# Performance work log

Hardware: AMD Instinct MI355X
Metric: run time of the kernel (lower is better)

## Reference

```python
import jax, jax.numpy as jnp
import numpy as np

N_NODES = 20000
N_EDGES = 640000
IN_NODE = 128
IN_EDGE = 16
HIDDEN = 64
OUT = 128
HEADS = 4
N_GRAPHS = 64
NEG_SLOPE = 0.2


def _glorot(key, shape):
    fan_in, fan_out = shape[0], shape[-1]
    s = jnp.sqrt(6.0 / (fan_in + fan_out)).astype(jnp.float32)
    return jax.random.uniform(key, shape, jnp.float32, -s, s)


def setup_inputs() -> dict:
    key = jax.random.key(0)
    ks = jax.random.split(key, 32)
    inp = {
        "x": jax.random.normal(ks[0], (N_NODES, IN_NODE), jnp.float32),
        "edge_attr": jax.random.normal(ks[1], (N_EDGES, IN_EDGE), jnp.float32),
        "edge_index": jax.random.randint(ks[2], (2, N_EDGES), 0, N_NODES),
        "batch": jnp.sort(jax.random.randint(ks[3], (N_NODES,), 0, N_GRAPHS)),
    }
    # layer dims: (in, out_per_head, concat)
    dims = [(IN_NODE, HIDDEN, True), (HIDDEN * HEADS, HIDDEN, True), (HIDDEN * HEADS, OUT, False)]
    k = 4
    for i, (cin, cout, concat) in enumerate(dims):
        hc = HEADS * cout
        inp[f"Wl{i}"] = _glorot(ks[k], (cin, hc)); k += 1
        inp[f"bl{i}"] = jnp.zeros((hc,), jnp.float32)
        inp[f"Wr{i}"] = _glorot(ks[k], (cin, hc)); k += 1
        inp[f"br{i}"] = jnp.zeros((hc,), jnp.float32)
        inp[f"We{i}"] = _glorot(ks[k], (IN_EDGE, hc)); k += 1
        inp[f"att{i}"] = _glorot(ks[k], (HEADS, cout)); k += 1
        inp[f"bias{i}"] = jnp.zeros((hc if concat else cout,), jnp.float32)
    return inp


def _gatv2_layer(x, edge_index, edge_attr, Wl, bl, Wr, br, We, att, bias, concat):
    """One PyG-style GATv2Conv layer with edge features."""
    H, C = att.shape
    N = x.shape[0]
    src, dst = edge_index[0], edge_index[1]
    xl = (x @ Wl + bl).reshape(N, H, C)  # messages from source
    xr = (x @ Wr + br).reshape(N, H, C)  # target query
    e = (edge_attr @ We).reshape(-1, H, C)
    m = jax.nn.leaky_relu(xl[src] + xr[dst] + e, NEG_SLOPE)  # [E,H,C]
    logits = jnp.einsum("ehc,hc->eh", m, att)  # [E,H]
    # scatter-softmax over edges grouped by destination node
    lmax = jax.ops.segment_max(logits, dst, num_segments=N)
    p = jnp.exp(logits - lmax[dst])
    denom = jax.ops.segment_sum(p, dst, num_segments=N)
    alpha = p / (denom[dst] + 1e-16)  # [E,H]
    out = jax.ops.segment_sum(alpha[:, :, None] * xl[src], dst, num_segments=N)  # [N,H,C]
    if concat:
        return out.reshape(N, H * C) + bias
    return out.mean(axis=1) + bias


def reference(x, edge_attr, edge_index, batch,
              Wl0, bl0, Wr0, br0, We0, att0, bias0,
              Wl1, bl1, Wr1, br1, We1, att1, bias1,
              Wl2, bl2, Wr2, br2, We2, att2, bias2):
    layers = [
        (Wl0, bl0, Wr0, br0, We0, att0, bias0, True),
        (Wl1, bl1, Wr1, br1, We1, att1, bias1, True),
        (Wl2, bl2, Wr2, br2, We2, att2, bias2, False),
    ]
    h = x
    for (Wl, bl, Wr, br, We, att, b, concat) in layers:
        h = _gatv2_layer(h, edge_index, edge_attr, Wl, bl, Wr, br, We, att, b, concat)
    # global max + mean pooling per graph
    x_max = jax.ops.segment_max(h, batch, num_segments=N_GRAPHS)
    s = jax.ops.segment_sum(h, batch, num_segments=N_GRAPHS)
    cnt = jax.ops.segment_sum(jnp.ones((h.shape[0], 1), h.dtype), batch, num_segments=N_GRAPHS)
    x_mean = s / jnp.maximum(cnt, 1.0)
    return jnp.concatenate([x_max, x_mean], axis=1)  # [G, 2*OUT]
```

## Files before the change

### kernel.cpp

```cpp
#include <hip/hip_runtime.h>

#define NB 8

__device__ __forceinline__ unsigned fmap(float f) {
  unsigned u = __float_as_uint(f);
  return (u & 0x80000000u) ? ~u : (u | 0x80000000u);
}
__device__ __forceinline__ float funmap(unsigned m) {
  unsigned u = (m & 0x80000000u) ? (m ^ 0x80000000u) : ~m;
  return __uint_as_float(u);
}

template <int K, int M>
__global__ __launch_bounds__(256) void node_gemm(
    const float* __restrict__ X, const float* __restrict__ W,
    const float* __restrict__ bias, float* __restrict__ Y) {
  constexpr int NPB = 16;
  constexpr int COLS4 = M / 4;
  constexpr int NG = 256 / COLS4;
  constexpr int RPN = NPB / NG;
  __shared__ float xs[NPB * K];
  const int tid = threadIdx.x;
  const int n0 = blockIdx.x * NPB;
  {
    const float4* X4 = reinterpret_cast<const float4*>(X + (size_t)n0 * K);
    float4* xs4 = reinterpret_cast<float4*>(xs);
    for (int i = tid; i < NPB * K / 4; i += 256) xs4[i] = X4[i];
  }
  __syncthreads();
  const int c4 = (tid % COLS4) * 4;
  const int r0 = (tid / COLS4) * RPN;
  float acc[RPN][4];
#pragma unroll
  for (int r = 0; r < RPN; ++r)
#pragma unroll
    for (int q = 0; q < 4; ++q) acc[r][q] = 0.f;

  for (int k = 0; k < K; k += 4) {
    float xv[RPN][4];
#pragma unroll
    for (int r = 0; r < RPN; ++r)
      *reinterpret_cast<float4*>(xv[r]) =
          *reinterpret_cast<const float4*>(&xs[(r0 + r) * K + k]);
#pragma unroll
    for (int j = 0; j < 4; ++j) {
      float wv[4];
      *reinterpret_cast<float4*>(wv) =
          *reinterpret_cast<const float4*>(&W[(size_t)(k + j) * M + c4]);
#pragma unroll
      for (int r = 0; r < RPN; ++r)
#pragma unroll
        for (int q = 0; q < 4; ++q)
          acc[r][q] = fmaf(xv[r][j], wv[q], acc[r][q]);
    }
  }
  float bv[4];
  *reinterpret_cast<float4*>(bv) = *reinterpret_cast<const float4*>(&bias[c4]);
#pragma unroll
  for (int r = 0; r < RPN; ++r) {
    float o[4];
#pragma unroll
    for (int q = 0; q < 4; ++q) o[q] = acc[r][q] + bv[q];
    *reinterpret_cast<float4*>(&Y[(size_t)(n0 + r0 + r) * M + c4]) =
        *reinterpret_cast<float4*>(o);
  }
}

__global__ void hist_b(const int* __restrict__ ei, int* __restrict__ kcnt,
                       int E, int bdiv) {
  int i = blockIdx.x * blockDim.x + threadIdx.x;
  if (i < E) atomicAdd(&kcnt[ei[E + i] * NB + ei[i] / bdiv], 1);
}

__global__ __launch_bounds__(1024) void blk_scan(
    const int* __restrict__ in, int* __restrict__ out1, int* __restrict__ bsum, int n) {
  __shared__ int buf[1024];
  const int tid = threadIdx.x;
  const int gid = blockIdx.x * 1024 + tid;
  int v = (gid < n) ? in[gid] : 0;
  buf[tid] = v;
  __syncthreads();
  for (int off = 1; off < 1024; off <<= 1) {
    int t = (tid >= off) ? buf[tid - off] : 0;
    __syncthreads();
    buf[tid] += t;
    __syncthreads();
  }
  if (gid < n) out1[gid] = buf[tid];
  if (tid == 1023) bsum[blockIdx.x] = buf[1023];
}

__global__ void scan_bsum(int* __restrict__ bsum, int nb) {
  if (blockIdx.x == 0 && threadIdx.x == 0) {
    int a = 0;
    for (int i = 0; i < nb; ++i) { a += bsum[i]; bsum[i] = a; }
  }
}

__global__ void add_off(int* __restrict__ kptr, const int* __restrict__ bsum, int n) {
  int gid = blockIdx.x * blockDim.x + threadIdx.x;
  if (gid == 0) kptr[0] = 0;
  if (gid < n) {
    int blk = gid >> 10;
    if (blk > 0) kptr[1 + gid] += bsum[blk - 1];
  }
}

__global__ void csr_fill_b(const int* __restrict__ ei, const int* __restrict__ kptr,
                           int* __restrict__ kfill, int* __restrict__ csr_src,
                           int* __restrict__ csr_eid, int E, int bdiv) {
  int i = blockIdx.x * blockDim.x + threadIdx.x;
  if (i < E) {
    int src = ei[i], dst = ei[E + i];
    int key = dst * NB + src / bdiv;
    int slot = kptr[key] + atomicAdd(&kfill[key], 1);
    csr_src[slot] = src;
    csr_eid[slot] = i;
  }
}

__global__ void ea_perm(const float* __restrict__ ea, const int* __restrict__ csr_eid,
                        float* __restrict__ ea_csr, int E) {
  int i = blockIdx.x * blockDim.x + threadIdx.x;
  if (i < E * 16) {
    int slot = i >> 4;
    ea_csr[i] = ea[((size_t)csr_eid[slot] << 4) + (i & 15)];
  }
}

template <int GS>
__device__ __forceinline__ void gat_edge_s(
    const float4 a, const float (&c)[16], const float4 xv,
    const float (&wef)[16][4], const float (&attv)[4],
    float& m, float& s, float (&acc)[4]) {
  float mv[4] = {a.x + xv.x, a.y + xv.y, a.z + xv.z, a.w + xv.w};
#pragma unroll
  for (int k = 0; k < 16; ++k) {
#pragma unroll
    for (int q = 0; q < 4; ++q) mv[q] = fmaf(c[k], wef[k][q], mv[q]);
  }
  float l = 0.f;
#pragma unroll
  for (int q = 0; q < 4; ++q) {
    const float v = fmaxf(mv[q], 0.2f * mv[q]);
    l = fmaf(v, attv[q], l);
  }
#pragma unroll
  for (int off = 1; off < GS; off <<= 1) l += __shfl_xor(l, off);
  const float nm = fmaxf(m, l);
  const float sc = __expf(m - nm);
  const float pe = __expf(l - nm);
  m = nm;
  s = fmaf(s, sc, pe);
  acc[0] = fmaf(pe, a.x, acc[0] * sc);
  acc[1] = fmaf(pe, a.y, acc[1] * sc);
  acc[2] = fmaf(pe, a.z, acc[2] * sc);
  acc[3] = fmaf(pe, a.w, acc[3] * sc);
}

template <int HCROW, int MODE>
__global__ __launch_bounds__(256) void fused_gat(
    const float* __restrict__ xl, const float* __restrict__ xr,
    const float* __restrict__ ea_csr, const float* __restrict__ We,
    const float* __restrict__ att, const float* __restrict__ bias,
    const int* __restrict__ kptr, const int* __restrict__ csr_src,
    float* __restrict__ out, int N, int colbase) {
  constexpr int C = HCROW / 4;
  constexpr int GS = C / 4;
  const int lane = threadIdx.x & 63;
  const int wslot = threadIdx.x >> 6;
  const int dst = blockIdx.x * 4 + wslot;
  if (dst >= N) return;

  float wef[16][4];
#pragma unroll
  for (int k = 0; k < 16; ++k)
    *reinterpret_cast<float4*>(wef[k]) =
        *reinterpret_cast<const float4*>(&We[k * HCROW + colbase + lane * 4]);
  const int col0 = colbase + lane * 4;
  const int head = col0 / C;
  float attv[4];
  *reinterpret_cast<float4*>(attv) =
      *reinterpret_cast<const float4*>(&att[head * C + (col0 % C)]);
  const float4* xl4 = reinterpret_cast<const float4*>(xl);
  const int rs4 = HCROW / 4;
  const int coff = col0 >> 2;
  const float4 xrv =
      reinterpret_cast<const float4*>(xr)[(size_t)dst * rs4 + coff];

  const int row0 = __builtin_amdgcn_readfirstlane(kptr[dst * NB]);
  const int rend = __builtin_amdgcn_readfirstlane(kptr[dst * NB + NB]);

  float m = -__builtin_inff(), s = 0.f;
  float acc[4] = {0.f, 0.f, 0.f, 0.f};

  if (row0 < rend) {
    const int last = rend - 1;
    const int s0 = csr_src[row0];
    const int s1 = csr_src[min(row0 + 1, last)];
    const int s2 = csr_src[min(row0 + 2, last)];
    const int s3 = csr_src[min(row0 + 3, last)];
    float4 a0 = xl4[(size_t)s0 * rs4 + coff];
    float4 a1 = xl4[(size_t)s1 * rs4 + coff];
    float4 a2 = xl4[(size_t)s2 * rs4 + coff];
    float4 a3 = xl4[(size_t)s3 * rs4 + coff];
    int sr0 = csr_src[min(row0 + 4, last)];
    int sr1 = csr_src[min(row0 + 5, last)];
    float c0[16], c1[16];
    {
      const float* e0 = ea_csr + (size_t)row0 * 16;
      const float* e1 = ea_csr + (size_t)min(row0 + 1, last) * 16;
#pragma unroll
      for (int k = 0; k < 16; ++k) { c0[k] = e0[k]; c1[k] = e1[k]; }
    }

    for (int p = row0; p < rend; p += 2) {
      const float4 na0 = xl4[(size_t)sr0 * rs4 + coff];
      const float4 na1 = xl4[(size_t)sr1 * rs4 + coff];
      const int nsr0 = csr_src[min(p + 6, last)];
      const int nsr1 = csr_src[min(p + 7, last)];
      float cn0[16], cn1[16];
      {
        const float* e0 = ea_csr + (size_t)min(p + 2, last) * 16;
        const float* e1 = ea_csr + (size_t)min(p + 3, last) * 16;
#pragma unroll
        for (int k = 0; k < 16; ++k) { cn0[k] = e0[k]; cn1[k] = e1[k]; }
      }
      gat_edge_s<GS>(a0, c0, xrv, wef, attv, m, s, acc);
      if (p + 1 < rend) gat_edge_s<GS>(a1, c1, xrv, wef, attv, m, s, acc);
      a0 = a2; a1 = a3; a2 = na0; a3 = na1;
      sr0 = nsr0; sr1 = nsr1;
#pragma unroll
      for (int k = 0; k < 16; ++k) { c0[k] = cn0[k]; c1[k] = cn1[k]; }
    }
  }

  const float inv = 1.f / (s + 1e-16f);
  float o[4];
  if (MODE == 0) {
    float bv[4];
    *reinterpret_cast<float4*>(bv) = *reinterpret_cast<const float4*>(&bias[col0]);
#pragma unroll
    for (int q = 0; q < 4; ++q) o[q] = fmaf(acc[q], inv, bv[q]);
    *reinterpret_cast<float4*>(&out[(size_t)dst * HCROW + col0]) =
        *reinterpret_cast<float4*>(o);
  } else {
#pragma unroll
    for (int q = 0; q < 4; ++q) {
      o[q] = acc[q] * inv;
      o[q] += __shfl_xor(o[q], 32);
    }
    if (lane < 32)
      *reinterpret_cast<float4*>(&out[(size_t)dst * 128 + lane * 4]) =
          *reinterpret_cast<float4*>(o);
  }
}

__global__ void pool_scatter(const float* __restrict__ hA, const float* __restrict__ hB,
                             const float* __restrict__ bias2, const int* __restrict__ batch,
                             unsigned* __restrict__ pmax, float* __restrict__ psum,
                             float* __restrict__ cnt, int N) {
  int idx = blockIdx.x * blockDim.x + threadIdx.x;
  if (idx >= N * 128) return;
  int n = idx >> 7, c = idx & 127;
  int g = batch[n];
  float v = 0.25f * (hA[idx] + hB[idx]) + bias2[c];
  atomicMax(&pmax[g * 128 + c], fmap(v));
  atomicAdd(&psum[g * 128 + c], v);
  if (c == 0) atomicAdd(&cnt[g], 1.f);
}

__global__ void pool_final(const unsigned* __restrict__ pmax, const float* __restrict__ psum,
                           const float* __restrict__ cnt, float* __restrict__ out) {
  int idx = blockIdx.x * blockDim.x + threadIdx.x;
  if (idx >= 64 * 128) return;
  int g = idx >> 7, c = idx & 127;
  float cg = cnt[g];
  out[g * 256 + c] = (cg > 0.f) ? funmap(pmax[idx]) : 0.f;
  out[g * 256 + 128 + c] = psum[idx] / fmaxf(cg, 1.f);
}

extern "C" void kernel_launch(void* const* d_in, const int* in_sizes, int n_in,
                              void* d_out, int out_size, void* d_ws, size_t ws_size,
                              hipStream_t stream) {
  const float* x     = (const float*)d_in[0];
  const float* ea    = (const float*)d_in[1];
  const int*   ei    = (const int*)d_in[2];
  const int*   batch = (const int*)d_in[3];
  const int N = in_sizes[0] / 128;
  const int E = in_sizes[2] / 2;
  const int NBINS = N * NB;
  const int bdiv = (N + NB - 1) / NB;

  const float* Wl[3]   = {(const float*)d_in[4],  (const float*)d_in[11], (const float*)d_in[18]};
  const float* blv[3]  = {(const float*)d_in[5],  (const float*)d_in[12], (const float*)d_in[19]};
  const float* Wr[3]   = {(const float*)d_in[6],  (const float*)d_in[13], (const float*)d_in[20]};
  const float* brv[3]  = {(const float*)d_in[7],  (const float*)d_in[14], (const float*)d_in[21]};
  const float* Wev[3]  = {(const float*)d_in[8],  (const float*)d_in[15], (const float*)d_in[22]};
  const float* attv[3] = {(const float*)d_in[9],  (const float*)d_in[16], (const float*)d_in[23]};
  const float* bias[3] = {(const float*)d_in[10], (const float*)d_in[17], (const float*)d_in[24]};

  float* ws = (float*)d_ws;
  float* xl     = ws;
  float* xr     = xl + (size_t)N * 512;
  float* ea_csr = xr + (size_t)N * 512;
  float* h      = ea_csr + (size_t)E * 16;
  int* kptr     = (int*)(h + (size_t)N * 256);
  int* csr_src  = kptr + (NBINS + 1);
  int* bsum     = csr_src + E;
  unsigned* pmax = (unsigned*)(bsum + 257);
  float* psum   = (float*)(pmax + 64 * 128);
  float* cnt    = psum + 64 * 128;
  int* csr_eid = (int*)h;
  int* kcnt    = csr_eid + E;
  int* kfill   = kcnt + NBINS;
  float* hsumA = h;
  float* hsumB = h + (size_t)N * 128;
  (void)n_in; (void)out_size; (void)ws_size;

  const int nodeBlocks = N / 16;
  const int edgeBlocks = (E + 255) / 256;
  const int scanBlocks = (NBINS + 1023) / 1024;
  const int gatBlocks = (N + 3) / 4;

  hipMemsetAsync(kcnt, 0, (size_t)2 * NBINS * sizeof(int), stream);
  hist_b<<<edgeBlocks, 256, 0, stream>>>(ei, kcnt, E, bdiv);
  blk_scan<<<scanBlocks, 1024, 0, stream>>>(kcnt, kptr + 1, bsum, NBINS);
  scan_bsum<<<1, 64, 0, stream>>>(bsum, scanBlocks);
  add_off<<<(NBINS + 255) / 256, 256, 0, stream>>>(kptr, bsum, NBINS);
  csr_fill_b<<<edgeBlocks, 256, 0, stream>>>(ei, kptr, kfill, csr_src, csr_eid, E, bdiv);
  ea_perm<<<(E * 16 + 255) / 256, 256, 0, stream>>>(ea, csr_eid, ea_csr, E);

  node_gemm<128, 256><<<nodeBlocks, 256, 0, stream>>>(x, Wl[0], blv[0], xl);
  node_gemm<128, 256><<<nodeBlocks, 256, 0, stream>>>(x, Wr[0], brv[0], xr);
  fused_gat<256, 0><<<gatBlocks, 256, 0, stream>>>(
      xl, xr, ea_csr, Wev[0], attv[0], bias[0], kptr, csr_src, h, N, 0);

  node_gemm<256, 256><<<nodeBlocks, 256, 0, stream>>>(h, Wl[1], blv[1], xl);
  node_gemm<256, 256><<<nodeBlocks, 256, 0, stream>>>(h, Wr[1], brv[1], xr);
  fused_gat<256, 0><<<gatBlocks, 256, 0, stream>>>(
      xl, xr, ea_csr, Wev[1], attv[1], bias[1], kptr, csr_src, h, N, 0);

  node_gemm<256, 512><<<nodeBlocks, 256, 0, stream>>>(h, Wl[2], blv[2], xl);
  node_gemm<256, 512><<<nodeBlocks, 256, 0, stream>>>(h, Wr[2], brv[2], xr);
  fused_gat<512, 1><<<gatBlocks, 256, 0, stream>>>(
      xl, xr, ea_csr, Wev[2], attv[2], bias[2], kptr, csr_src, hsumA, N, 0);
  fused_gat<512, 1><<<gatBlocks, 256, 0, stream>>>(
      xl, xr, ea_csr, Wev[2], attv[2], bias[2], kptr, csr_src, hsumB, N, 256);

  hipMemsetAsync(pmax, 0, (size_t)(64 * 128 * 2 + 64) * sizeof(float), stream);
  pool_scatter<<<(N * 128 + 255) / 256, 256, 0, stream>>>(hsumA, hsumB, bias[2], batch,
                                                          pmax, psum, cnt, N);
  pool_final<<<(64 * 128 + 255) / 256, 256, 0, stream>>>(pmax, psum, cnt, (float*)d_out);
}
```

Before: 1.119 ms.

## Replace atomic pooling with per-graph segmented reduction and merge final GAT launches

Per-node atomic max/sum pooling is replaced by a per-graph reduction. A small kernel finds each graph's node range from the sorted batch array, then one block per graph reduces its contiguous rows. This removes heavy atomic contention on 64x128 targets and drops the pool_final launch. The two column-half launches of the last GAT layer are also merged into one grid of twice the size. The pooling relies on batch being sorted, and 64 blocks give limited parallelism for the reduction.

```diff
diff --git a/kernel.cpp b/kernel.cpp
--- a/kernel.cpp
+++ b/kernel.cpp
@@ -1,15 +1,6 @@
 #include <hip/hip_runtime.h>
 
 #define NB 8
-
-__device__ __forceinline__ unsigned fmap(float f) {
-  unsigned u = __float_as_uint(f);
-  return (u & 0x80000000u) ? ~u : (u | 0x80000000u);
-}
-__device__ __forceinline__ float funmap(unsigned m) {
-  unsigned u = (m & 0x80000000u) ? (m ^ 0x80000000u) : ~m;
-  return __uint_as_float(u);
-}
 
 template <int K, int M>
 __global__ __launch_bounds__(256) void node_gemm(
@@ -128,6 +119,16 @@
   }
 }
 
+__global__ void graph_bounds(const int* __restrict__ batch, int* __restrict__ gstart,
+                             int* __restrict__ gend, int N) {
+  int i = blockIdx.x * blockDim.x + threadIdx.x;
+  if (i < N) {
+    int g = batch[i];
+    atomicMin(&gstart[g], i);
+    atomicMax(&gend[g], i + 1);
+  }
+}
+
 template <int GS>
 __device__ __forceinline__ void gat_edge_s(
     const float4 a, const float (&c)[16], const float4 xv,
@@ -164,12 +165,19 @@
     const float* __restrict__ ea_csr, const float* __restrict__ We,
     const float* __restrict__ att, const float* __restrict__ bias,
     const int* __restrict__ kptr, const int* __restrict__ csr_src,
-    float* __restrict__ out, int N, int colbase) {
+    float* __restrict__ out, float* __restrict__ outB, int N) {
   constexpr int C = HCROW / 4;
   constexpr int GS = C / 4;
   const int lane = threadIdx.x & 63;
   const int wslot = threadIdx.x >> 6;
-  const int dst = blockIdx.x * 4 + wslot;
+  int bx = blockIdx.x;
+  int colbase = 0;
+  float* o_ptr = out;
+  if (MODE == 1) {
+    const int gb = gridDim.x >> 1;
+    if (bx >= gb) { bx -= gb; colbase = 256; o_ptr = outB; }
+  }
+  const int dst = bx * 4 + wslot;
   if (dst >= N) return;
 
   float wef[16][4];
@@ -242,7 +250,7 @@
     *reinterpret_cast<float4*>(bv) = *reinterpret_cast<const float4*>(&bias[col0]);
 #pragma unroll
     for (int q = 0; q < 4; ++q) o[q] = fmaf(acc[q], inv, bv[q]);
-    *reinterpret_cast<float4*>(&out[(size_t)dst * HCROW + col0]) =
+    *reinterpret_cast<float4*>(&o_ptr[(size_t)dst * HCROW + col0]) =
         *reinterpret_cast<float4*>(o);
   } else {
 #pragma unroll
@@ -251,33 +259,36 @@
       o[q] += __shfl_xor(o[q], 32);
     }
     if (lane < 32)
-      *reinterpret_cast<float4*>(&out[(size_t)dst * 128 + lane * 4]) =
+      *reinterpret_cast<float4*>(&o_ptr[(size_t)dst * 128 + lane * 4]) =
           *reinterpret_cast<float4*>(o);
   }
 }
 
-__global__ void pool_scatter(const float* __restrict__ hA, const float* __restrict__ hB,
-                             const float* __restrict__ bias2, const int* __restrict__ batch,
-                             unsigned* __restrict__ pmax, float* __restrict__ psum,
-                             float* __restrict__ cnt, int N) {
-  int idx = blockIdx.x * blockDim.x + threadIdx.x;
-  if (idx >= N * 128) return;
-  int n = idx >> 7, c = idx & 127;
-  int g = batch[n];
-  float v = 0.25f * (hA[idx] + hB[idx]) + bias2[c];
-  atomicMax(&pmax[g * 128 + c], fmap(v));
-  atomicAdd(&psum[g * 128 + c], v);
-  if (c == 0) atomicAdd(&cnt[g], 1.f);
-}
-
-__global__ void pool_final(const unsigned* __restrict__ pmax, const float* __restrict__ psum,
-                           const float* __restrict__ cnt, float* __restrict__ out) {
-  int idx = blockIdx.x * blockDim.x + threadIdx.x;
-  if (idx >= 64 * 128) return;
-  int g = idx >> 7, c = idx & 127;
-  float cg = cnt[g];
-  out[g * 256 + c] = (cg > 0.f) ? funmap(pmax[idx]) : 0.f;
-  out[g * 256 + 128 + c] = psum[idx] / fmaxf(cg, 1.f);
+__global__ __launch_bounds__(256) void pool_graph(
+    const float* __restrict__ hA, const float* __restrict__ hB,
+    const float* __restrict__ bias2, const int* __restrict__ gstart,
+    const int* __restrict__ gend, float* __restrict__ out) {
+  const int g = blockIdx.x;
+  const int c = threadIdx.x & 127;
+  const int sub = threadIdx.x >> 7;
+  const int s0 = gstart[g], e0 = gend[g];
+  const float b = bias2[c];
+  float mx = -__builtin_inff(), sm = 0.f;
+  for (int n = s0 + sub; n < e0; n += 2) {
+    const float v = fmaf(0.25f, hA[(size_t)n * 128 + c] + hB[(size_t)n * 128 + c], b);
+    mx = fmaxf(mx, v);
+    sm += v;
+  }
+  __shared__ float smx[128], ssm[128];
+  if (sub) { smx[c] = mx; ssm[c] = sm; }
+  __syncthreads();
+  if (!sub) {
+    mx = fmaxf(mx, smx[c]);
+    sm += ssm[c];
+    const int cnt = e0 - s0;
+    out[g * 256 + c] = (cnt > 0) ? mx : 0.f;
+    out[g * 256 + 128 + c] = sm / fmaxf((float)cnt, 1.f);
+  }
 }
 
 extern "C" void kernel_launch(void* const* d_in, const int* in_sizes, int n_in,
@@ -308,9 +319,8 @@
   int* kptr     = (int*)(h + (size_t)N * 256);
   int* csr_src  = kptr + (NBINS + 1);
   int* bsum     = csr_src + E;
-  unsigned* pmax = (unsigned*)(bsum + 257);
-  float* psum   = (float*)(pmax + 64 * 128);
-  float* cnt    = psum + 64 * 128;
+  int* gstart   = bsum + 257;
+  int* gend     = gstart + 64;
   int* csr_eid = (int*)h;
   int* kcnt    = csr_eid + E;
   int* kfill   = kcnt + NBINS;
@@ -324,7 +334,10 @@
   const int gatBlocks = (N + 3) / 4;
 
   hipMemsetAsync(kcnt, 0, (size_t)2 * NBINS * sizeof(int), stream);
+  hipMemsetAsync(gstart, 0x7f, 64 * sizeof(int), stream);
+  hipMemsetAsync(gend, 0, 64 * sizeof(int), stream);
   hist_b<<<edgeBlocks, 256, 0, stream>>>(ei, kcnt, E, bdiv);
+  graph_bounds<<<(N + 255) / 256, 256, 0, stream>>>(batch, gstart, gend, N);
   blk_scan<<<scanBlocks, 1024, 0, stream>>>(kcnt, kptr + 1, bsum, NBINS);
   scan_bsum<<<1, 64, 0, stream>>>(bsum, scanBlocks);
   add_off<<<(NBINS + 255) / 256, 256, 0, stream>>>(kptr, bsum, NBINS);
@@ -334,22 +347,17 @@
   node_gemm<128, 256><<<nodeBlocks, 256, 0, stream>>>(x, Wl[0], blv[0], xl);
   node_gemm<128, 256><<<nodeBlocks, 256, 0, stream>>>(x, Wr[0], brv[0], xr);
   fused_gat<256, 0><<<gatBlocks, 256, 0, stream>>>(
-      xl, xr, ea_csr, Wev[0], attv[0], bias[0], kptr, csr_src, h, N, 0);
+      xl, xr, ea_csr, Wev[0], attv[0], bias[0], kptr, csr_src, h, nullptr, N);
 
   node_gemm<256, 256><<<nodeBlocks, 256, 0, stream>>>(h, Wl[1], blv[1], xl);
   node_gemm<256, 256><<<nodeBlocks, 256, 0, stream>>>(h, Wr[1], brv[1], xr);
   fused_gat<256, 0><<<gatBlocks, 256, 0, stream>>>(
-      xl, xr, ea_csr, Wev[1], attv[1], bias[1], kptr, csr_src, h, N, 0);
+      xl, xr, ea_csr, Wev[1], attv[1], bias[1], kptr, csr_src, h, nullptr, N);
 
   node_gemm<256, 512><<<nodeBlocks, 256, 0, stream>>>(h, Wl[2], blv[2], xl);
   node_gemm<256, 512><<<nodeBlocks, 256, 0, stream>>>(h, Wr[2], brv[2], xr);
-  fused_gat<512, 1><<<gatBlocks, 256, 0, stream>>>(
-      xl, xr, ea_csr, Wev[2], attv[2], bias[2], kptr, csr_src, hsumA, N, 0);
-  fused_gat<512, 1><<<gatBlocks, 256, 0, stream>>>(
-      xl, xr, ea_csr, Wev[2], attv[2], bias[2], kptr, csr_src, hsumB, N, 256);
-
-  hipMemsetAsync(pmax, 0, (size_t)(64 * 128 * 2 + 64) * sizeof(float), stream);
-  pool_scatter<<<(N * 128 + 255) / 256, 256, 0, stream>>>(hsumA, hsumB, bias[2], batch,
-                                                          pmax, psum, cnt, N);
-  pool_final<<<(64 * 128 + 255) / 256, 256, 0, stream>>>(pmax, psum, cnt, (float*)d_out);
-}
+  fused_gat<512, 1><<<2 * gatBlocks, 256, 0, stream>>>(
+      xl, xr, ea_csr, Wev[2], attv[2], bias[2], kptr, csr_src, hsumA, hsumB, N);
+
+  pool_graph<<<64, 256, 0, stream>>>(hsumA, hsumB, bias[2], gstart, gend, (float*)d_out);
+}
```

New measurement: 1.107 ms. Within noise of the previous version (-1.0%).
